# Kernel optimization log

Measured on AMD Instinct MI355X. Metric: run time of the kernel, lower is better.

## Reference

```python
import jax, jax.numpy as jnp
import numpy as np
from jax import lax


def _spectral_topk_filter(X, k):
    # X: complex (B, Freq, F). Keep top-k magnitude freqs per (batch, feature).
    Xt = jnp.transpose(X, (0, 2, 1))  # (B, F, Freq)
    mag = jnp.abs(Xt)
    _, idx = lax.top_k(mag, k)  # (B, F, k)
    vals = jnp.take_along_axis(Xt, idx, axis=-1)
    B, F, _ = Xt.shape
    bi = jnp.arange(B)[:, None, None]
    fi = jnp.arange(F)[None, :, None]
    filt = jnp.zeros_like(Xt).at[bi, fi, idx].set(vals)
    return jnp.transpose(filt, (0, 2, 1))  # (B, Freq, F)


def _hamming_periodic(W):
    # matches torch.hamming_window(W) default (periodic=True)
    n = jnp.arange(W, dtype=jnp.float32)
    return 0.54 - 0.46 * jnp.cos(2.0 * jnp.pi * n / W)


def setup_inputs() -> dict:
    key = jax.random.key(0)
    x = jax.random.normal(key, (32, 4096, 128), dtype=jnp.float32)
    return {"x": x, "window_size": 25, "k": 16}


def reference(x, window_size, k):
    B, T, F = x.shape
    W = window_size
    half = W // 2

    # spectral filter: rfft -> keep top-k freqs -> irfft
    X = jnp.fft.rfft(x, axis=1)
    Xf = _spectral_topk_filter(X, k)
    xf = jnp.fft.irfft(Xf, axis=1).astype(x.dtype)  # (B, T, F)

    # flip-padding as in the torch module
    left = xf[:, :half, :][:, ::-1, :]
    right = xf[:, -half:, :][:, ::-1, :]
    xp = jnp.concatenate([left, xf, right], axis=1)  # (B, T + 2*half, F)

    # sliding hamming-window average == depthwise 1D correlation (no kernel flip,
    # matching the elementwise multiply in the original loop)
    w = _hamming_periodic(W).astype(x.dtype)
    xr = jnp.transpose(xp, (0, 2, 1)).reshape(B * F, 1, -1)  # (B*F, 1, Tp)
    out = lax.conv_general_dilated(xr, w[None, None, :], (1,), 'VALID')  # (B*F, 1, T)
    out = out.reshape(B, F, T).transpose(0, 2, 1) / jnp.sum(w)
    return out
```

## Files before the change

kernel.cpp:

```cpp
#include <hip/hip_runtime.h>
#include <math.h>


#define NN     4096
#define LOGN   12
#define NT     256
#define EPT    16
#define KTOP   16
#define WSZ    25
#define HALFW  12
#define FDIM   128
#define BATCH  32
#define RECL   88
#define TT     128
#define TWO_PI 6.283185307179586f

__device__ __forceinline__ int swz(int a) { return a + (a >> 5); }

#define CMUL(r, i, wr_, wi_) { float _r = (r); (r) = _r * (wr_) - (i) * (wi_); (i) = _r * (wi_) + (i) * (wr_); }
#define MULNI(r, i)          { float _r = (r); (r) = (i); (i) = -_r; }

__device__ __forceinline__ void cs_phase(int ph, float& c, float& s)
{
    const float rev = (float)ph * (1.0f / (float)NN);
    s = __builtin_amdgcn_sinf(rev);
    c = __builtin_amdgcn_cosf(rev);
}

__device__ __forceinline__ void dft16(float (&zr)[16], float (&zi)[16])
{
    const float C1 = 0.92387953251128674f;
    const float S1 = 0.38268343236508978f;
    const float R2 = 0.70710678118654752f;
    float yr[16], yi[16];
    #pragma unroll
    for (int n2 = 0; n2 < 4; ++n2) {
        float ar = zr[n2],      ai = zi[n2];
        float br = zr[4 + n2],  bi = zi[4 + n2];
        float cr = zr[8 + n2],  ci = zi[8 + n2];
        float dr = zr[12 + n2], di = zi[12 + n2];
        float t0r = ar + cr, t0i = ai + ci;
        float t1r = ar - cr, t1i = ai - ci;
        float t2r = br + dr, t2i = bi + di;
        float t3r = br - dr, t3i = bi - di;
        yr[n2]      = t0r + t2r;  yi[n2]      = t0i + t2i;
        yr[4 + n2]  = t1r + t3i;  yi[4 + n2]  = t1i - t3r;
        yr[8 + n2]  = t0r - t2r;  yi[8 + n2]  = t0i - t2i;
        yr[12 + n2] = t1r - t3i;  yi[12 + n2] = t1i + t3r;
    }
    CMUL(yr[5],  yi[5],  C1, -S1);
    CMUL(yr[6],  yi[6],  R2, -R2);
    CMUL(yr[7],  yi[7],  S1, -C1);
    CMUL(yr[9],  yi[9],  R2, -R2);
    MULNI(yr[10], yi[10]);
    CMUL(yr[11], yi[11], -R2, -R2);
    CMUL(yr[13], yi[13], S1, -C1);
    CMUL(yr[14], yi[14], -R2, -R2);
    CMUL(yr[15], yi[15], -C1, S1);
    #pragma unroll
    for (int k1 = 0; k1 < 4; ++k1) {
        float ar = yr[k1 * 4 + 0], ai = yi[k1 * 4 + 0];
        float br = yr[k1 * 4 + 1], bi = yi[k1 * 4 + 1];
        float cr = yr[k1 * 4 + 2], ci = yi[k1 * 4 + 2];
        float dr = yr[k1 * 4 + 3], di = yi[k1 * 4 + 3];
        float t0r = ar + cr, t0i = ai + ci;
        float t1r = ar - cr, t1i = ai - ci;
        float t2r = br + dr, t2i = bi + di;
        float t3r = br - dr, t3i = bi - di;
        zr[k1]      = t0r + t2r;  zi[k1]      = t0i + t2i;
        zr[4 + k1]  = t1r + t3i;  zi[4 + k1]  = t1i - t3r;
        zr[8 + k1]  = t0r - t2r;  zi[8 + k1]  = t0i - t2i;
        zr[12 + k1] = t1r - t3i;  zi[12 + k1] = t1i + t3r;
    }
}

__global__ __launch_bounds__(256)
void transpose_kernel(const float* __restrict__ in, float* __restrict__ out,
                      int R, int C)
{
    __shared__ float tile[64][65];
    const int b = blockIdx.z;
    const float* pin  = in  + (size_t)b * R * C;
    float*       pout = out + (size_t)b * R * C;
    const int r0 = blockIdx.y * 64, c0 = blockIdx.x * 64;
    const int tc4 = (threadIdx.x & 15) * 4;
    const int tr  = threadIdx.x >> 4;
    #pragma unroll
    for (int i = 0; i < 4; ++i) {
        int r = tr + i * 16;
        float4 v = *(const float4*)&pin[(size_t)(r0 + r) * C + c0 + tc4];
        tile[r][tc4 + 0] = v.x; tile[r][tc4 + 1] = v.y;
        tile[r][tc4 + 2] = v.z; tile[r][tc4 + 3] = v.w;
    }
    __syncthreads();
    #pragma unroll
    for (int i = 0; i < 4; ++i) {
        int r = tr + i * 16;
        float4 v;
        v.x = tile[tc4 + 0][r]; v.y = tile[tc4 + 1][r];
        v.z = tile[tc4 + 2][r]; v.w = tile[tc4 + 3][r];
        *(float4*)&pout[(size_t)(c0 + r) * R + r0 + tc4] = v;
    }
}

__global__ __launch_bounds__(NT, 4)
void spectral_fft_kernel(float* __restrict__ ws)
{
    __shared__ float s_re[NN + (NN >> 5)];
    __shared__ float s_im[NN + (NN >> 5)];
    __shared__ float s_w[WSZ];
    __shared__ float s_wsum;
    __shared__ float s_rv[8];
    __shared__ int   s_rk[8];
    __shared__ int   s_kf[KTOP];
    __shared__ float s_kr[KTOP];
    __shared__ float s_ki[KTOP];
    __shared__ float s_vr[KTOP];
    __shared__ float s_vi[KTOP];
    __shared__ float s_cd2[KTOP];
    __shared__ float s_edge[2 * HALFW];
    __shared__ float s_dl[2 * HALFW];

    const int tid = threadIdx.x;
    float* chan = ws + (size_t)blockIdx.x * NN;

    if (tid < WSZ)
        s_w[tid] = 0.54f - 0.46f * cosf(TWO_PI * (float)tid / (float)WSZ);

    float zr[16], zi[16];
    #pragma unroll
    for (int r = 0; r < 16; ++r) { zr[r] = chan[tid + (r << 8)]; zi[r] = 0.0f; }

    dft16(zr, zi);

    if (tid == 0) {
        float a = 0.0f;
        for (int i = 0; i < WSZ; ++i) a += s_w[i];
        s_wsum = a;
    }

    {
        float sn, cs;
        sincosf(-TWO_PI * (float)tid / (float)NN, &sn, &cs);
        float dr = cs, di = sn;
        float wr = dr, wi = di;
        #pragma unroll
        for (int u = 1; u < 16; ++u) {
            CMUL(zr[u], zi[u], wr, wi);
            float nr = wr * dr - wi * di; wi = wr * di + wi * dr; wr = nr;
        }
        #pragma unroll
        for (int u = 0; u < 16; ++u) {
            int a = swz(tid + (u << 8));
            s_re[a] = zr[u]; s_im[a] = zi[u];
        }
    }
    __syncthreads();

    {
        const int p = tid & 15;
        const int b0 = ((tid >> 4) << 8) + p;
        #pragma unroll
        for (int r = 0; r < 16; ++r) {
            int a = swz(b0 + (r << 4));
            zr[r] = s_re[a]; zi[r] = s_im[a];
        }
        dft16(zr, zi);
        float sn, cs;
        sincosf(-TWO_PI * (float)(p << 4) / (float)NN, &sn, &cs);
        float dr = cs, di = sn;
        float wr = dr, wi = di;
        #pragma unroll
        for (int u = 1; u < 16; ++u) {
            CMUL(zr[u], zi[u], wr, wi);
            float nr = wr * dr - wi * di; wi = wr * di + wi * dr; wr = nr;
        }
        #pragma unroll
        for (int u = 0; u < 16; ++u) {
            int a = swz(b0 + (u << 4));
            s_re[a] = zr[u]; s_im[a] = zi[u];
        }
    }
    __syncthreads();

    {
        #pragma unroll
        for (int r = 0; r < 16; ++r) {
            int a = swz((tid << 4) + r);
            zr[r] = s_re[a]; zi[r] = s_im[a];
        }
        dft16(zr, zi);
    }

    const int fbase = ((tid & 15) << 4) | (tid >> 4);
    float mg[9];
    float lmax = -1.0f; int lk = 0x7fffffff;
    #pragma unroll
    for (int u = 0; u < 9; ++u) {
        float v = zr[u] * zr[u] + zi[u] * zi[u];
        if (u == 8 && fbase != 0) v = -1.0f;
        mg[u] = v;
        if (v > lmax) { lmax = v; lk = (u << 8) + fbase; }
    }

    for (int r = 0; r < KTOP; ++r) {
        float bv = lmax; int bk = lk;
        #pragma unroll
        for (int off = 32; off > 0; off >>= 1) {
            float ov = __shfl_down(bv, off);
            int   ok = __shfl_down(bk, off);
            if (ov > bv || (ov == bv && ok < bk)) { bv = ov; bk = ok; }
        }
        const int buf = (r & 1) << 2;
        if ((tid & 63) == 0) { s_rv[buf + (tid >> 6)] = bv; s_rk[buf + (tid >> 6)] = bk; }
        __syncthreads();
        bv = s_rv[buf]; bk = s_rk[buf];
        #pragma unroll
        for (int w2 = 1; w2 < 4; ++w2) {
            float ov = s_rv[buf + w2]; int ok = s_rk[buf + w2];
            if (ov > bv || (ov == bv && ok < bk)) { bv = ov; bk = ok; }
        }
        if (lmax == bv && lk == bk) {
            const int uw = bk >> 8;
            s_kf[r] = bk;
            #pragma unroll
            for (int u2 = 0; u2 < 9; ++u2) {
                if (u2 == uw) { s_kr[r] = zr[u2]; s_ki[r] = zi[u2]; mg[u2] = -1.0f; }
            }
            lmax = -1.0f; lk = 0x7fffffff;
            #pragma unroll
            for (int u2 = 0; u2 < 9; ++u2) {
                float v = mg[u2];
                if (v > lmax) { lmax = v; lk = (u2 << 8) + fbase; }
            }
        }
    }
    __syncthreads();

    if (tid < 2 * HALFW) {
        const int te = (tid < HALFW) ? tid : (NN - 2 * HALFW + tid);
        float a = 0.0f;
        for (int r = 0; r < KTOP; ++r) {
            const int fj = s_kf[r];
            float vr = s_kr[r], vi = s_ki[r];
            if (fj == 0 || fj == NN / 2) { vi = 0.0f; }
            else { vr *= 2.0f; vi *= 2.0f; }
            float c, s;
            cs_phase((fj * te) & (NN - 1), c, s);
            a += vr * c - vi * s;
        }
        s_edge[tid] = a * (1.0f / (float)NN);
    }
    if (tid >= 64 && tid < 64 + KTOP) {
        const int r = tid - 64;
        const int fj = s_kf[r];
        float vr = s_kr[r], vi = s_ki[r];
        float sc;
        if (fj == 0 || fj == NN / 2) { vi = 0.0f; sc = 1.0f; }
        else                         { sc = 2.0f; }
        float cr, ci, dc, ds;
        cs_phase((-HALFW * fj) & (NN - 1), cr, ci);
        cs_phase(fj, dc, ds);
        float hr = 0.0f, hi = 0.0f;
        for (int i = 0; i < WSZ; ++i) {
            const float wv = s_w[i];
            hr += wv * cr; hi += wv * ci;
            float nc = cr * dc - ci * ds;
            ci = ci * dc + cr * ds;
            cr = nc;
        }
        const float scale = sc / ((float)NN * s_wsum);
        s_vr[r]  = (vr * hr - vi * hi) * scale;
        s_vi[r]  = (vr * hi + vi * hr) * scale;
        s_cd2[r] = dc + dc;
    }
    __syncthreads();

    if (tid == 0) {
        const float rinv = 1.0f / s_wsum;
        for (int t = 0; t < HALFW; ++t) {
            float d = 0.0f;
            for (int i = 0; t + i < HALFW; ++i)
                d += s_w[i] * (s_edge[HALFW - 1 - t - i] - s_edge[HALFW + t + i]);
            s_dl[t] = d * rinv;
        }
        for (int j = 0; j < HALFW; ++j) {
            float d = 0.0f;
            for (int i = 2 * HALFW - j; i < WSZ; ++i)
                d += s_w[i] * (s_edge[4 * HALFW - 1 - j - i] - s_edge[j + i - 2 * HALFW]);
            s_dl[HALFW + j] = d * rinv;
        }
    }
    __syncthreads();

    if (tid < RECL) {
        float v;
        if      (tid < 16) v = s_vr[tid];
        else if (tid < 32) v = s_vi[tid - 16];
        else if (tid < 48) v = s_cd2[tid - 32];
        else if (tid < 64) v = (float)s_kf[tid - 48];
        else               v = s_dl[tid - 64];
        chan[tid] = v;
    }
}

__global__ __launch_bounds__(NT, 3)
void spectral_recon_kernel(const float* __restrict__ ws, float* __restrict__ out)
{
    __shared__ float s_c[FDIM * (RECL + 1)];

    const int tid = threadIdx.x;
    const int tb  = blockIdx.x * TT;
    const int b   = blockIdx.y;
    const int chB = b * FDIM;

    #pragma unroll
    for (int k = 0; k < (FDIM * RECL) / NT; ++k) {
        int idx = tid + k * NT;
        int ch  = idx / RECL;
        int j   = idx - ch * RECL;
        s_c[ch * (RECL + 1) + j] = ws[(size_t)(chB + ch) * NN + j];
    }
    __syncthreads();

    const int m  = tid & 31;
    const int tq = tid >> 5;
    const int t0 = tb + tq * 16;

    float acc[4][16];
    #pragma unroll
    for (int c = 0; c < 4; ++c)
        #pragma unroll
        for (int i = 0; i < 16; ++i) acc[c][i] = 0.0f;

    for (int r = 0; r < KTOP; ++r) {
        #pragma unroll
        for (int c = 0; c < 4; ++c) {
            const float* rec = &s_c[(c * 32 + m) * (RECL + 1)];
            const float vr  = rec[r];
            const float vi  = rec[16 + r];
            const float cd2 = rec[32 + r];
            const int   fj  = (int)rec[48 + r];
            const int   p0  = (fj * t0) & (NN - 1);
            float c0, s0, cm, sm;
            cs_phase(p0, c0, s0);
            cs_phase((p0 - fj) & (NN - 1), cm, sm);
            float g1 = vr * c0 - vi * s0;
            float g0 = vr * cm - vi * sm;
            #pragma unroll
            for (int i = 0; i < 16; ++i) {
                acc[c][i] += g1;
                const float gn = __builtin_fmaf(cd2, g1, -g0);
                g0 = g1; g1 = gn;
            }
        }
    }

    #pragma unroll
    for (int c = 0; c < 4; ++c) {
        const int ch = c * 32 + m;
        const float* rec = &s_c[ch * (RECL + 1)];
        if (tb == 0 && tq == 0) {
            #pragma unroll
            for (int i = 0; i < HALFW; ++i) acc[c][i] += rec[64 + i];
        }
        if (tb == NN - TT && tq == 7) {
            #pragma unroll
            for (int i = 4; i < 16; ++i) acc[c][i] += rec[76 + (i - 4)];
        }
        const size_t obase = ((size_t)b * NN + t0) * FDIM + ch;
        #pragma unroll
        for (int i = 0; i < 16; ++i)
            out[obase + (size_t)i * FDIM] = acc[c][i];
    }
}

__global__ __launch_bounds__(NT, 3)
void spectral_filter_fallback(const float* __restrict__ x, float* __restrict__ out)
{
    __shared__ float s_re[NN + (NN >> 5)];
    __shared__ float s_im[NN];
    __shared__ float s_tw[NN];
    __shared__ float s_w[WSZ];
    __shared__ float s_wsum;
    __shared__ float s_rv[NT / 64];
    __shared__ int   s_ri[NT / 64];
    __shared__ int   s_kf[KTOP];
    __shared__ float s_kr[KTOP];
    __shared__ float s_ki[KTOP];

    const int tid = threadIdx.x;
    const int c   = blockIdx.x;
    const int b   = c >> 7;
    const int f   = c & (FDIM - 1);
    const size_t base = (size_t)b * NN * FDIM + f;

    if (tid < WSZ)
        s_w[tid] = 0.54f - 0.46f * cosf(TWO_PI * (float)tid / (float)WSZ);

    for (int i = tid; i < NN / 2; i += NT) {
        float sn, cs;
        sincosf(-TWO_PI * (float)i / (float)NN, &sn, &cs);
        s_tw[i]          = cs;
        s_tw[i + NN / 2] = sn;
    }

    #pragma unroll
    for (int i = 0; i < EPT; ++i) {
        int j = tid + i * NT;
        int t = (int)(__brev((unsigned)j) >> (32 - LOGN));
        s_re[j] = x[base + (size_t)t * FDIM];
        s_im[j] = 0.0f;
    }
    __syncthreads();

    if (tid == 0) {
        float a = 0.0f;
        for (int i = 0; i < WSZ; ++i) a += s_w[i];
        s_wsum = a;
    }

    for (int s = 1; s <= LOGN; ++s) {
        const int half = 1 << (s - 1);
        const int tsh  = LOGN - s;
        #pragma unroll
        for (int i = 0; i < EPT / 2; ++i) {
            int j  = tid + i * NT;
            int p  = j & (half - 1);
            int i0 = ((j >> (s - 1)) << s) + p;
            int i1 = i0 + half;
            int q  = p << tsh;
            float wr = s_tw[q], wi = s_tw[q + NN / 2];
            float ar = s_re[i0], ai = s_im[i0];
            float br = s_re[i1], bi = s_im[i1];
            float tr = br * wr - bi * wi;
            float ti = br * wi + bi * wr;
            s_re[i0] = ar + tr;  s_im[i0] = ai + ti;
            s_re[i1] = ar - tr;  s_im[i1] = ai - ti;
        }
        __syncthreads();
    }

    for (int i = tid; i < NN / 2 + 1; i += NT) {
        float rr = s_re[i], ii = s_im[i];
        s_tw[i] = rr * rr + ii * ii;
    }
    __syncthreads();

    for (int r = 0; r < KTOP; ++r) {
        float best = -1.0f; int bidx = 0x7fffffff;
        for (int i = tid; i < NN / 2 + 1; i += NT) {
            float v = s_tw[i];
            if (v > best) { best = v; bidx = i; }
        }
        #pragma unroll
        for (int off = 32; off > 0; off >>= 1) {
            float ov = __shfl_down(best, off);
            int   oi = __shfl_down(bidx, off);
            if (ov > best || (ov == best && oi < bidx)) { best = ov; bidx = oi; }
        }
        const int wid = tid >> 6;
        if ((tid & 63) == 0) { s_rv[wid] = best; s_ri[wid] = bidx; }
        __syncthreads();
        if (tid == 0) {
            float bv = s_rv[0]; int bx = s_ri[0];
            #pragma unroll
            for (int w2 = 1; w2 < NT / 64; ++w2) {
                float ov = s_rv[w2]; int oi = s_ri[w2];
                if (ov > bv || (ov == bv && oi < bx)) { bv = ov; bx = oi; }
            }
            s_kf[r] = bx;
            s_kr[r] = s_re[bx];
            s_ki[r] = s_im[bx];
            s_tw[bx] = -1.0f;
        }
        __syncthreads();
    }

    const int t0 = tid * EPT;
    float xf[EPT];
    #pragma unroll
    for (int i = 0; i < EPT; ++i) xf[i] = 0.0f;

    for (int r = 0; r < KTOP; ++r) {
        const int fj = s_kf[r];
        float vr = s_kr[r], vi = s_ki[r];
        float sc = 2.0f;
        if (fj == 0 || fj == NN / 2) { sc = 1.0f; vi = 0.0f; }
        vr *= sc; vi *= sc;
        const int ph0 = (fj * t0) & (NN - 1);
        float c0, s0, dc, ds;
        sincosf((float)ph0 * (TWO_PI / (float)NN), &s0, &c0);
        sincosf((float)fj  * (TWO_PI / (float)NN), &ds, &dc);
        float cr = c0, ci = s0;
        #pragma unroll
        for (int i = 0; i < EPT; ++i) {
            xf[i] += vr * cr - vi * ci;
            float nc = cr * dc - ci * ds;
            ci = ci * dc + cr * ds;
            cr = nc;
        }
    }
    __syncthreads();

    #pragma unroll
    for (int i = 0; i < EPT; ++i)
        s_re[swz(t0 + i)] = xf[i] * (1.0f / (float)NN);
    __syncthreads();

    float win[EPT + WSZ - 1];
    #pragma unroll
    for (int i = 0; i < EPT + WSZ - 1; ++i) {
        int a = t0 + i - HALFW;
        if (a < 0)        a = -1 - a;
        else if (a >= NN) a = 2 * NN - 1 - a;
        win[i] = s_re[swz(a)];
    }

    const float rinv = 1.0f / s_wsum;
    float acc[EPT];
    #pragma unroll
    for (int t = 0; t < EPT; ++t) acc[t] = 0.0f;
    #pragma unroll
    for (int i = 0; i < WSZ; ++i) {
        const float wv = s_w[i];
        #pragma unroll
        for (int t = 0; t < EPT; ++t) acc[t] += win[t + i] * wv;
    }
    #pragma unroll
    for (int t = 0; t < EPT; ++t)
        out[base + (size_t)(t0 + t) * FDIM] = acc[t] * rinv;
}

extern "C" void kernel_launch(void* const* d_in, const int* in_sizes, int n_in,
                              void* d_out, int out_size, void* d_ws, size_t ws_size,
                              hipStream_t stream)
{
    const float* x = (const float*)d_in[0];
    float* out = (float*)d_out;
    const size_t need = (size_t)BATCH * FDIM * NN * sizeof(float);
    if (ws_size >= need) {
        float* ws = (float*)d_ws;
        transpose_kernel<<<dim3(FDIM / 64, NN / 64, BATCH), 256, 0, stream>>>(x, ws, NN, FDIM);
        spectral_fft_kernel<<<dim3(BATCH * FDIM), NT, 0, stream>>>(ws);
        spectral_recon_kernel<<<dim3(NN / TT, BATCH), NT, 0, stream>>>(ws, out);
    } else {
        spectral_filter_fallback<<<dim3(BATCH * FDIM), NT, 0, stream>>>(x, out);
    }
}
```

Baseline: 248.6 us.

## Drop transpose kernel, read strided input directly in FFT with XCD-aware block mapping

Removes the separate transpose pass and makes the FFT kernel load each channel directly from the (B,T,F) input with stride FDIM. Block indices are remapped so consecutive blocks on the same XCD cover neighbouring features and can share cache lines. The per-channel records are stored compactly (RECL floats) instead of at NN stride. The recon kernel's shared tile shrinks to 64 fields so occupancy can rise to 4, with edge corrections read from global memory. The risk is that the strided global loads in the FFT kernel are uncoalesced and rely on L2 reuse across blocks.

```diff
diff --git a/kernel.cpp b/kernel.cpp
--- a/kernel.cpp
+++ b/kernel.cpp
@@ -74,37 +74,8 @@
     }
 }
 
-__global__ __launch_bounds__(256)
-void transpose_kernel(const float* __restrict__ in, float* __restrict__ out,
-                      int R, int C)
-{
-    __shared__ float tile[64][65];
-    const int b = blockIdx.z;
-    const float* pin  = in  + (size_t)b * R * C;
-    float*       pout = out + (size_t)b * R * C;
-    const int r0 = blockIdx.y * 64, c0 = blockIdx.x * 64;
-    const int tc4 = (threadIdx.x & 15) * 4;
-    const int tr  = threadIdx.x >> 4;
-    #pragma unroll
-    for (int i = 0; i < 4; ++i) {
-        int r = tr + i * 16;
-        float4 v = *(const float4*)&pin[(size_t)(r0 + r) * C + c0 + tc4];
-        tile[r][tc4 + 0] = v.x; tile[r][tc4 + 1] = v.y;
-        tile[r][tc4 + 2] = v.z; tile[r][tc4 + 3] = v.w;
-    }
-    __syncthreads();
-    #pragma unroll
-    for (int i = 0; i < 4; ++i) {
-        int r = tr + i * 16;
-        float4 v;
-        v.x = tile[tc4 + 0][r]; v.y = tile[tc4 + 1][r];
-        v.z = tile[tc4 + 2][r]; v.w = tile[tc4 + 3][r];
-        *(float4*)&pout[(size_t)(c0 + r) * R + r0 + tc4] = v;
-    }
-}
-
 __global__ __launch_bounds__(NT, 4)
-void spectral_fft_kernel(float* __restrict__ ws)
+void spectral_fft_kernel(const float* __restrict__ x, float* __restrict__ ws)
 {
     __shared__ float s_re[NN + (NN >> 5)];
     __shared__ float s_im[NN + (NN >> 5)];
@@ -122,14 +93,19 @@
     __shared__ float s_dl[2 * HALFW];
 
     const int tid = threadIdx.x;
-    float* chan = ws + (size_t)blockIdx.x * NN;
+
+    const int p  = blockIdx.x;
+    const int wg = ((p & 7) << 9) + (p >> 3);
+    const int b  = wg >> 7;
+    const int f  = wg & (FDIM - 1);
+    const float* xc = x + (size_t)b * NN * FDIM + f;
 
     if (tid < WSZ)
         s_w[tid] = 0.54f - 0.46f * cosf(TWO_PI * (float)tid / (float)WSZ);
 
     float zr[16], zi[16];
     #pragma unroll
-    for (int r = 0; r < 16; ++r) { zr[r] = chan[tid + (r << 8)]; zi[r] = 0.0f; }
+    for (int r = 0; r < 16; ++r) { zr[r] = xc[(tid + (r << 8)) * FDIM]; zi[r] = 0.0f; }
 
     dft16(zr, zi);
 
@@ -158,8 +134,8 @@
     __syncthreads();
 
     {
-        const int p = tid & 15;
-        const int b0 = ((tid >> 4) << 8) + p;
+        const int pp = tid & 15;
+        const int b0 = ((tid >> 4) << 8) + pp;
         #pragma unroll
         for (int r = 0; r < 16; ++r) {
             int a = swz(b0 + (r << 4));
@@ -167,7 +143,7 @@
         }
         dft16(zr, zi);
         float sn, cs;
-        sincosf(-TWO_PI * (float)(p << 4) / (float)NN, &sn, &cs);
+        sincosf(-TWO_PI * (float)(pp << 4) / (float)NN, &sn, &cs);
         float dr = cs, di = sn;
         float wr = dr, wi = di;
         #pragma unroll
@@ -300,14 +276,14 @@
         else if (tid < 48) v = s_cd2[tid - 32];
         else if (tid < 64) v = (float)s_kf[tid - 48];
         else               v = s_dl[tid - 64];
-        chan[tid] = v;
+        ws[(size_t)wg * RECL + tid] = v;
     }
 }
 
-__global__ __launch_bounds__(NT, 3)
+__global__ __launch_bounds__(NT, 4)
 void spectral_recon_kernel(const float* __restrict__ ws, float* __restrict__ out)
 {
-    __shared__ float s_c[FDIM * (RECL + 1)];
+    __shared__ float s_c[FDIM * 65];
 
     const int tid = threadIdx.x;
     const int tb  = blockIdx.x * TT;
@@ -315,11 +291,11 @@
     const int chB = b * FDIM;
 
     #pragma unroll
-    for (int k = 0; k < (FDIM * RECL) / NT; ++k) {
-        int idx = tid + k * NT;
-        int ch  = idx / RECL;
-        int j   = idx - ch * RECL;
-        s_c[ch * (RECL + 1) + j] = ws[(size_t)(chB + ch) * NN + j];
+    for (int k = 0; k < (FDIM * 64) / NT; ++k) {
+        int idx = tid + (k << 8);
+        int ch  = idx >> 6;
+        int j   = idx & 63;
+        s_c[ch * 65 + j] = ws[(size_t)(chB + ch) * RECL + j];
     }
     __syncthreads();
 
@@ -336,7 +312,7 @@
     for (int r = 0; r < KTOP; ++r) {
         #pragma unroll
         for (int c = 0; c < 4; ++c) {
-            const float* rec = &s_c[(c * 32 + m) * (RECL + 1)];
+            const float* rec = &s_c[(c * 32 + m) * 65];
             const float vr  = rec[r];
             const float vi  = rec[16 + r];
             const float cd2 = rec[32 + r];
@@ -359,14 +335,15 @@
     #pragma unroll
     for (int c = 0; c < 4; ++c) {
         const int ch = c * 32 + m;
-        const float* rec = &s_c[ch * (RECL + 1)];
         if (tb == 0 && tq == 0) {
             #pragma unroll
-            for (int i = 0; i < HALFW; ++i) acc[c][i] += rec[64 + i];
+            for (int i = 0; i < HALFW; ++i)
+                acc[c][i] += ws[(size_t)(chB + ch) * RECL + 64 + i];
         }
         if (tb == NN - TT && tq == 7) {
             #pragma unroll
-            for (int i = 4; i < 16; ++i) acc[c][i] += rec[76 + (i - 4)];
+            for (int i = 4; i < 16; ++i)
+                acc[c][i] += ws[(size_t)(chB + ch) * RECL + 76 + (i - 4)];
         }
         const size_t obase = ((size_t)b * NN + t0) * FDIM + ch;
         #pragma unroll
@@ -538,11 +515,10 @@
 {
     const float* x = (const float*)d_in[0];
     float* out = (float*)d_out;
-    const size_t need = (size_t)BATCH * FDIM * NN * sizeof(float);
+    const size_t need = (size_t)BATCH * FDIM * RECL * sizeof(float);
     if (ws_size >= need) {
         float* ws = (float*)d_ws;
-        transpose_kernel<<<dim3(FDIM / 64, NN / 64, BATCH), 256, 0, stream>>>(x, ws, NN, FDIM);
-        spectral_fft_kernel<<<dim3(BATCH * FDIM), NT, 0, stream>>>(ws);
+        spectral_fft_kernel<<<dim3(BATCH * FDIM), NT, 0, stream>>>(x, ws);
         spectral_recon_kernel<<<dim3(NN / TT, BATCH), NT, 0, stream>>>(ws, out);
     } else {
         spectral_filter_fallback<<<dim3(BATCH * FDIM), NT, 0, stream>>>(x, out);
```

Result: no change. 249.1 us (+0.2%).
